# Kernel optimization log

Hardware: AMD Instinct MI355X
Metric: run time of the kernel (lower is better)

## Reference

```python
import jax, jax.numpy as jnp
import numpy as np

N = 100_000   # nodes
E = 1_600_000 # edges
F = 128       # node_feature_dim
H = 128       # hidden_dim
A = 32        # action_dim
G = 64        # graphs in batch


def setup_inputs() -> dict:
    key = jax.random.key(0)
    ks = jax.random.split(key, 12)
    s = 0.05
    return {
        "x": jax.random.normal(ks[0], (N, F), jnp.float32),
        "edge_index": jax.random.randint(ks[1], (2, E), 0, N, dtype=jnp.int32),
        "batch": jnp.sort(jax.random.randint(ks[2], (N,), 0, G, dtype=jnp.int32)),
        "W1": jax.random.normal(ks[3], (F, H), jnp.float32) * s,
        "b1": jnp.zeros((H,), jnp.float32),
        "W2": jax.random.normal(ks[4], (H, H), jnp.float32) * s,
        "b2": jnp.zeros((H,), jnp.float32),
        "Wa": jax.random.normal(ks[5], (H, A), jnp.float32) * s,
        "ba": jnp.zeros((A,), jnp.float32),
        "Wv": jax.random.normal(ks[6], (H, 1), jnp.float32) * s,
        "bv": jnp.zeros((1,), jnp.float32),
        "log_std": jnp.zeros((A,), jnp.float32),
    }


def reference(x, edge_index, batch, W1, b1, W2, b2, Wa, ba, Wv, bv, log_std):
    src, dst = edge_index[0], edge_index[1]
    # GCN symmetric norm with self-loops: deg_i = 1 + #incoming edges
    deg = jax.ops.segment_sum(jnp.ones((E,), x.dtype), dst, num_segments=N) + 1.0
    dinv = deg ** -0.5  # [N]

    def gcn(h, W, b):
        h = h @ W                                   # [N,H] dense transform first (as PyG GCNConv)
        msg = h[src] * dinv[src, None]              # gather + src norm
        agg = jax.ops.segment_sum(msg, dst, num_segments=N) * dinv[:, None]
        agg = agg + h * (dinv * dinv)[:, None]      # self-loop contribution
        return agg + b

    h = jax.nn.relu(gcn(x, W1, b1))
    h = jax.nn.relu(gcn(h, W2, b2))

    # global_mean_pool over graph segments
    counts = jax.ops.segment_sum(jnp.ones((N,), h.dtype), batch, num_segments=G)
    pooled = jax.ops.segment_sum(h, batch, num_segments=G) / jnp.maximum(counts, 1.0)[:, None]

    action_mean = pooled @ Wa + ba                  # [G,A]
    value = (pooled @ Wv + bv)[:, 0]                # [G]
    return action_mean, jnp.exp(log_std), value
```

## Files before the change

kernel.cpp:

```cpp
#include <hip/hip_runtime.h>
#include <hip/hip_bf16.h>

#define FDIM 128
#define HDIM 128
#define ADIM 32
#define BSH 6
#define BWD 64
#define CHUNK 8192
#define MAXNB 2048
#define CSRCAP 2048

#define CP(p) ((((p) & 7) << 4) | ((p) >> 3))

typedef short v8s __attribute__((ext_vector_type(8)));
typedef float v4f __attribute__((ext_vector_type(4)));
typedef float v2f __attribute__((ext_vector_type(2)));

static __device__ __forceinline__ float bflo(unsigned int u) {
    return __builtin_bit_cast(float, u << 16);
}
static __device__ __forceinline__ float bfhi(unsigned int u) {
    return __builtin_bit_cast(float, u & 0xffff0000u);
}
static __device__ __forceinline__ unsigned int bfpack(float a, float b) {
    unsigned int ua = __builtin_bit_cast(unsigned int, a);
    unsigned int ub = __builtin_bit_cast(unsigned int, b);
    ua += 0x7fffu + ((ua >> 16) & 1u);
    ub += 0x7fffu + ((ub >> 16) & 1u);
    return (ua >> 16) | (ub & 0xffff0000u);
}

#if defined(__has_builtin) && __has_builtin(__builtin_amdgcn_cvt_pk_f32_fp8) && \
    __has_builtin(__builtin_amdgcn_cvt_pk_fp8_f32)
#define FP8_HW 1
#endif

static __device__ __forceinline__ v2f fp8_dec_lo(unsigned int u) {
#ifdef FP8_HW
    return __builtin_amdgcn_cvt_pk_f32_fp8(u, false);
#else
    v2f r;
    #pragma unroll
    for (int i = 0; i < 2; ++i) {
        unsigned b = (u >> (8 * i)) & 0xffu;
        unsigned s = b >> 7, e = (b >> 3) & 0xfu, m = b & 7u;
        float v = (e == 0) ? (float)m * 0.001953125f
                           : __builtin_bit_cast(float, ((e + 120u) << 23) | (m << 20));
        r[i] = s ? -v : v;
    }
    return r;
#endif
}
static __device__ __forceinline__ v2f fp8_dec_hi(unsigned int u) {
#ifdef FP8_HW
    return __builtin_amdgcn_cvt_pk_f32_fp8(u, true);
#else
    return fp8_dec_lo(u >> 16);
#endif
}

#ifndef FP8_HW
static __device__ __forceinline__ unsigned int fp8_enc1(float x) {
    unsigned s = __builtin_bit_cast(unsigned, x) >> 31;
    float ax = fabsf(x);
    if (ax > 448.f) return (s << 7) | 0x7Eu;
    if (ax < 0.0009765625f) return s << 7;
    int e2 = (int)((__builtin_bit_cast(unsigned, ax) >> 23) & 0xff) - 127;
    int qe = (e2 < -6 ? -6 : e2) - 3;
    float q = __builtin_bit_cast(float, (unsigned)((qe + 127) << 23));
    float r = rintf(ax / q) * q;
    if (r > 448.f) return (s << 7) | 0x7Eu;
    if (r < 0.001953125f) return s << 7;
    unsigned ub = __builtin_bit_cast(unsigned, r);
    int re = (int)((ub >> 23) & 0xff) - 127;
    if (re < -6) {
        unsigned m = (unsigned)rintf(r * 512.f);
        return (s << 7) | m;
    }
    return (s << 7) | ((unsigned)(re + 7) << 3) | ((ub >> 20) & 7u);
}
#endif

static __device__ __forceinline__ unsigned int fp8x4_enc(float a, float b, float c, float d) {
#ifdef FP8_HW
    int p = __builtin_amdgcn_cvt_pk_fp8_f32(a, b, 0, false);
    p = __builtin_amdgcn_cvt_pk_fp8_f32(c, d, p, true);
    return (unsigned int)p;
#else
    return fp8_enc1(a) | (fp8_enc1(b) << 8) | (fp8_enc1(c) << 16) | (fp8_enc1(d) << 24);
#endif
}

__global__ __launch_bounds__(256) void block_hist_setup(const int* __restrict__ dst,
                                                        int* __restrict__ hist,
                                                        int E, int NB, int NBLK,
                                                        const float* __restrict__ W1,
                                                        const float* __restrict__ W2,
                                                        const float* __restrict__ b1,
                                                        const float* __restrict__ b2,
                                                        unsigned short* __restrict__ wsw1,
                                                        unsigned short* __restrict__ wsw2,
                                                        float* __restrict__ pb1,
                                                        float* __restrict__ pb2,
                                                        const int* __restrict__ batch,
                                                        int* __restrict__ gstart,
                                                        float* __restrict__ pooled,
                                                        unsigned int* __restrict__ zrow,
                                                        int n, int G) {
    __shared__ int h[MAXNB];
    const int tid = threadIdx.x;
    if (blockIdx.x >= (unsigned)NBLK) {
        const int role = blockIdx.x - NBLK;
        if (role == 0) {
            for (int idx = tid; idx < 16384; idx += 256) {
                int nn = idx >> 7, k = idx & 127;
                wsw1[idx] = (unsigned short)(bfpack(W1[k * 128 + nn], 0.f) & 0xffffu);
                wsw2[idx] = (unsigned short)(bfpack(W2[CP(k) * 128 + nn], 0.f) & 0xffffu);
            }
            if (tid < 128) {
                pb1[tid] = b1[CP(tid)];
                pb2[tid] = b2[CP(tid)];
            }
        } else if (role == 1) {
            if (tid <= G) {
                int lo = 0, hi = n;
                while (lo < hi) { int mid = (lo + hi) >> 1; if (batch[mid] < tid) lo = mid + 1; else hi = mid; }
                gstart[tid] = lo;
            }
        } else {
            for (int i = tid; i < G * 128; i += 256) pooled[i] = 0.f;
            if (tid < 32) zrow[tid] = 0u;
        }
        return;
    }
    for (int i = tid; i < NB; i += 256) h[i] = 0;
    __syncthreads();
    const int base = blockIdx.x * CHUNK;
    int lim = base + CHUNK; if (lim > E) lim = E;
    for (int i = base + tid; i < lim; i += 256) atomicAdd(&h[dst[i] >> BSH], 1);
    __syncthreads();
    int* hrow = hist + (size_t)blockIdx.x * NB;
    for (int b = tid; b < NB; b += 256) hrow[b] = h[b];
}

__global__ void scanA(const int* __restrict__ hist, int* __restrict__ excl,
                      int* __restrict__ bsum, int M, int NB, int NBLK) {
    __shared__ int tmp[256];
    const int t = threadIdx.x;
    const int idx = blockIdx.x * 2048 + t * 8;
    int v[8], s = 0;
    #pragma unroll
    for (int i = 0; i < 8; ++i) {
        int p = idx + i;
        v[i] = (p < M) ? hist[(size_t)(p % NBLK) * NB + (p / NBLK)] : 0;
        s += v[i];
    }
    tmp[t] = s;
    __syncthreads();
    for (int off = 1; off < 256; off <<= 1) {
        int x = (t >= off) ? tmp[t - off] : 0;
        __syncthreads();
        tmp[t] += x;
        __syncthreads();
    }
    int run = tmp[t] - s;
    #pragma unroll
    for (int i = 0; i < 8; ++i) {
        int p = idx + i;
        if (p < M) excl[p] = run;
        run += v[i];
    }
    if (t == 255) bsum[blockIdx.x] = tmp[255];
}

__global__ void scanB(int* __restrict__ bsum, int nb) {
    __shared__ int tmp[256];
    const int t = threadIdx.x;
    int s = (t < nb) ? bsum[t] : 0;
    tmp[t] = s;
    __syncthreads();
    for (int off = 1; off < 256; off <<= 1) {
        int x = (t >= off) ? tmp[t - off] : 0;
        __syncthreads();
        tmp[t] += x;
        __syncthreads();
    }
    if (t < nb) bsum[t] = tmp[t] - s;
}

__global__ __launch_bounds__(256) void bucket_scatter(const int* __restrict__ src,
                                                      const int* __restrict__ dst,
                                                      const int* __restrict__ excl,
                                                      const int* __restrict__ bsum,
                                                      unsigned int* __restrict__ packed,
                                                      int E, int NB, int NBLK) {
    __shared__ int cur[MAXNB];
    const int tid = threadIdx.x;
    const int blk = blockIdx.x;
    for (int b = tid; b < NB; b += 256) {
        size_t p = (size_t)b * NBLK + blk;
        cur[b] = excl[p] + bsum[p >> 11];
    }
    __syncthreads();
    const int base = blk * CHUNK;
    int lim = base + CHUNK; if (lim > E) lim = E;
    for (int i = base + tid; i < lim; i += 256) {
        int d = dst[i];
        int s = src[i];
        int pos = atomicAdd(&cur[d >> BSH], 1);
        packed[pos] = (unsigned)s | ((unsigned)(d & (BWD - 1)) << 26);
    }
}

__global__ __launch_bounds__(256) void bucket_to_csr(const unsigned int* __restrict__ packed,
                                                     const int* __restrict__ excl,
                                                     const int* __restrict__ bsum,
                                                     int* __restrict__ rowptr,
                                                     int* __restrict__ pdeg,
                                                     float* __restrict__ dinv,
                                                     int* __restrict__ col,
                                                     int E, int N, int NB, int NBLK) {
    __shared__ int cnt[BWD];
    __shared__ int offs[BWD];
    __shared__ int ovf;
    const int b = blockIdx.x;
    const int tid = threadIdx.x;
    size_t p0 = (size_t)b * NBLK;
    const int base = excl[p0] + bsum[p0 >> 11];
    int next;
    if (b + 1 < NB) {
        size_t p1 = (size_t)(b + 1) * NBLK;
        next = excl[p1] + bsum[p1 >> 11];
    } else {
        next = E;
    }
    if (tid < BWD) cnt[tid] = 0;
    if (tid == 0) ovf = 0;
    __syncthreads();
    for (int i = base + tid; i < next; i += 256) atomicAdd(&cnt[packed[i] >> 26], 1);
    __syncthreads();
    const int rc = (tid < BWD) ? cnt[tid] : 0;
    if (tid == 0) {
        int run = 0;
        for (int j = 0; j < BWD; ++j) { offs[j] = run; run += (cnt[j] + 7) & ~7; }
        if (run > CSRCAP) {
            ovf = 1;
            run = 0;
            for (int j = 0; j < BWD; ++j) { offs[j] = run; run += cnt[j]; }
        }
    }
    __syncthreads();
    const int cbase = b * CSRCAP;
    if (tid < BWD) {
        int node = (b << BSH) + tid;
        if (node < N) {
            int pd = ovf ? rc : ((rc + 7) & ~7);
            int st = cbase + offs[tid];
            rowptr[node] = st;
            pdeg[node] = pd;
            dinv[node] = rsqrtf((float)rc + 1.0f);
            for (int k = rc; k < pd; ++k) col[st + k] = N;
        }
        cnt[tid] = offs[tid];
    }
    __syncthreads();
    for (int i = base + tid; i < next; i += 256) {
        unsigned int u = packed[i];
        int j = u >> 26;
        int pos = cbase + atomicAdd(&cnt[j], 1);
        col[pos] = (int)(u & 0x03ffffffu);
    }
}

template <bool BF16IN>
__global__ __launch_bounds__(256, 4) void gemm_mfma(const void* __restrict__ Xv,
                                                    const unsigned short* __restrict__ wsw,
                                                    const float* __restrict__ rowscale,
                                                    uint2* __restrict__ Out, int n) {
    __shared__ char sW[32768];
    const int tid = threadIdx.x;
    const int w = tid >> 6;
    const int lane = tid & 63;
    const int q = lane >> 4;
    const int m15 = lane & 15;
    const int rbase = blockIdx.x * 64;

    const int arow = rbase + w * 16 + m15;
    const int srow = (arow < n) ? arow : (n - 1);

    uint4 ta[4];
    float4 tf[8];
    if (BF16IN) {
        const unsigned short* xr = (const unsigned short*)Xv + (size_t)srow * 128 + q * 8;
        #pragma unroll
        for (int kk = 0; kk < 4; ++kk) ta[kk] = *(const uint4*)(xr + kk * 32);
    } else {
        const float* xr = (const float*)Xv + (size_t)srow * 128 + q * 8;
        #pragma unroll
        for (int kk = 0; kk < 4; ++kk) {
            tf[2 * kk]     = *(const float4*)(xr + kk * 32);
            tf[2 * kk + 1] = *(const float4*)(xr + kk * 32 + 4);
        }
    }

    #pragma unroll
    for (int it = 0; it < 8; ++it) {
        int fi = it * 256 + tid;
        uint4 v = ((const uint4*)wsw)[fi];
        *(uint4*)(sW + ((fi * 16) ^ (((fi >> 4) & 7) << 4))) = v;
    }
    __syncthreads();

    v8s a[4];
    if (BF16IN) {
        #pragma unroll
        for (int kk = 0; kk < 4; ++kk) a[kk] = __builtin_bit_cast(v8s, ta[kk]);
    } else {
        #pragma unroll
        for (int kk = 0; kk < 4; ++kk) {
            uint4 p;
            p.x = bfpack(tf[2 * kk].x, tf[2 * kk].y);
            p.y = bfpack(tf[2 * kk].z, tf[2 * kk].w);
            p.z = bfpack(tf[2 * kk + 1].x, tf[2 * kk + 1].y);
            p.w = bfpack(tf[2 * kk + 1].z, tf[2 * kk + 1].w);
            a[kk] = __builtin_bit_cast(v8s, p);
        }
    }

    const int swz = (m15 & 7) << 4;
    v8s bcur[4], bnxt[4];
    #pragma unroll
    for (int kk = 0; kk < 4; ++kk)
        bcur[kk] = *(const v8s*)(sW + (((m15 * 16 + kk * 4 + q) * 16) ^ swz));

    v4f acc[8];
    #pragma unroll
    for (int nt = 0; nt < 8; ++nt) acc[nt] = (v4f){0.f, 0.f, 0.f, 0.f};

    #pragma unroll
    for (int nt = 0; nt < 8; ++nt) {
        if (nt < 7) {
            #pragma unroll
            for (int kk = 0; kk < 4; ++kk)
                bnxt[kk] = *(const v8s*)(sW +
                    (((((nt + 1) * 16 + m15) * 16 + kk * 4 + q) * 16) ^ swz));
        }
        #pragma unroll
        for (int kk = 0; kk < 4; ++kk)
            acc[nt] = __builtin_amdgcn_mfma_f32_16x16x32_bf16(a[kk], bcur[kk], acc[nt], 0, 0, 0);
        #pragma unroll
        for (int kk = 0; kk < 4; ++kk) bcur[kk] = bnxt[kk];
    }

    #pragma unroll
    for (int reg = 0; reg < 4; ++reg) {
        int row = rbase + w * 16 + q * 4 + reg;
        if (row < n) {
            float sc = rowscale[row];
            unsigned int d0 = fp8x4_enc(acc[0][reg] * sc, acc[1][reg] * sc,
                                        acc[2][reg] * sc, acc[3][reg] * sc);
            unsigned int d1 = fp8x4_enc(acc[4][reg] * sc, acc[5][reg] * sc,
                                        acc[6][reg] * sc, acc[7][reg] * sc);
            Out[(size_t)row * 16 + m15] = make_uint2(d0, d1);
        }
    }
}

__global__ __launch_bounds__(256) void gather_fused(const unsigned int* __restrict__ T32,
                                                    const int* __restrict__ rowptr,
                                                    const int* __restrict__ pdeg,
                                                    const int* __restrict__ col,
                                                    const float* __restrict__ dinv,
                                                    const float* __restrict__ pbias,
                                                    uint2* __restrict__ H, int n) {
    const int wave = (blockIdx.x * 256 + threadIdx.x) >> 6;
    const int d = wave * 2 + ((threadIdx.x >> 5) & 1);
    const int hl = threadIdx.x & 31;
    if (d >= n) return;
    int e = rowptr[d];
    const int end = e + pdeg[d];

    v2f sl0 = {0.f, 0.f}, sh0 = {0.f, 0.f}, sl1 = {0.f, 0.f}, sh1 = {0.f, 0.f};

    if ((e & 1) && e < end) {
        unsigned int u = T32[(size_t)col[e] * 32 + hl];
        sl0 += fp8_dec_lo(u); sh0 += fp8_dec_hi(u);
        ++e;
    }
    for (; e + 7 < end; e += 8) {
        int2 p01 = *(const int2*)(col + e);
        int2 p23 = *(const int2*)(col + e + 2);
        int2 p45 = *(const int2*)(col + e + 4);
        int2 p67 = *(const int2*)(col + e + 6);
        unsigned int u0 = T32[(size_t)p01.x * 32 + hl];
        unsigned int u1 = T32[(size_t)p01.y * 32 + hl];
        unsigned int u2 = T32[(size_t)p23.x * 32 + hl];
        unsigned int u3 = T32[(size_t)p23.y * 32 + hl];
        unsigned int u4 = T32[(size_t)p45.x * 32 + hl];
        unsigned int u5 = T32[(size_t)p45.y * 32 + hl];
        unsigned int u6 = T32[(size_t)p67.x * 32 + hl];
        unsigned int u7 = T32[(size_t)p67.y * 32 + hl];
        sl0 += fp8_dec_lo(u0); sh0 += fp8_dec_hi(u0);
        sl1 += fp8_dec_lo(u1); sh1 += fp8_dec_hi(u1);
        sl0 += fp8_dec_lo(u2); sh0 += fp8_dec_hi(u2);
        sl1 += fp8_dec_lo(u3); sh1 += fp8_dec_hi(u3);
        sl0 += fp8_dec_lo(u4); sh0 += fp8_dec_hi(u4);
        sl1 += fp8_dec_lo(u5); sh1 += fp8_dec_hi(u5);
        sl0 += fp8_dec_lo(u6); sh0 += fp8_dec_hi(u6);
        sl1 += fp8_dec_lo(u7); sh1 += fp8_dec_hi(u7);
    }
    for (; e + 1 < end; e += 2) {
        int2 p = *(const int2*)(col + e);
        unsigned int u0 = T32[(size_t)p.x * 32 + hl];
        unsigned int u1 = T32[(size_t)p.y * 32 + hl];
        sl0 += fp8_dec_lo(u0); sh0 += fp8_dec_hi(u0);
        sl1 += fp8_dec_lo(u1); sh1 += fp8_dec_hi(u1);
    }
    if (e < end) {
        unsigned int u = T32[(size_t)col[e] * 32 + hl];
        sl0 += fp8_dec_lo(u); sh0 += fp8_dec_hi(u);
    }

    unsigned int su = T32[(size_t)d * 32 + hl];
    sl0 += fp8_dec_lo(su); sh0 += fp8_dec_hi(su);
    v2f sl = sl0 + sl1, sh = sh0 + sh1;

    const float di = dinv[d];
    const float4 bv = ((const float4*)pbias)[hl];
    float o0 = fmaxf(fmaf(sl.x, di, bv.x), 0.f);
    float o1 = fmaxf(fmaf(sl.y, di, bv.y), 0.f);
    float o2 = fmaxf(fmaf(sh.x, di, bv.z), 0.f);
    float o3 = fmaxf(fmaf(sh.y, di, bv.w), 0.f);
    uint2 o;
    o.x = bfpack(o0, o1);
    o.y = bfpack(o2, o3);
    H[(size_t)d * 32 + hl] = o;
}

__global__ __launch_bounds__(256) void gather_pool(const unsigned int* __restrict__ T32,
                                                   const int* __restrict__ rowptr,
                                                   const int* __restrict__ pdeg,
                                                   const int* __restrict__ col,
                                                   const float* __restrict__ dinv,
                                                   const float* __restrict__ pbias,
                                                   float* __restrict__ pooled,
                                                   const int* __restrict__ batch,
                                                   int n) {
    __shared__ float pacc[256];
    const int tid = threadIdx.x;
    const int hw = tid >> 5;
    const int hl = tid & 31;
    const int base = blockIdx.x * 64;
    pacc[tid] = 0.f;
    const int g0 = batch[base < n ? base : (n - 1)];
    __syncthreads();

    const float4 bv = ((const float4*)pbias)[hl];
    float r0a = 0.f, r0b = 0.f, r0c = 0.f, r0d = 0.f;
    float r1a = 0.f, r1b = 0.f, r1c = 0.f, r1d = 0.f;

    for (int it = 0; it < 8; ++it) {
        const int d = base + hw * 8 + it;
        if (d < n) {
            int e = rowptr[d];
            const int end = e + pdeg[d];

            v2f sl0 = {0.f, 0.f}, sh0 = {0.f, 0.f}, sl1 = {0.f, 0.f}, sh1 = {0.f, 0.f};

            if ((e & 1) && e < end) {
                unsigned int u = T32[(size_t)col[e] * 32 + hl];
                sl0 += fp8_dec_lo(u); sh0 += fp8_dec_hi(u);
                ++e;
            }
            for (; e + 7 < end; e += 8) {
                int2 p01 = *(const int2*)(col + e);
                int2 p23 = *(const int2*)(col + e + 2);
                int2 p45 = *(const int2*)(col + e + 4);
                int2 p67 = *(const int2*)(col + e + 6);
                unsigned int u0 = T32[(size_t)p01.x * 32 + hl];
                unsigned int u1 = T32[(size_t)p01.y * 32 + hl];
                unsigned int u2 = T32[(size_t)p23.x * 32 + hl];
                unsigned int u3 = T32[(size_t)p23.y * 32 + hl];
                unsigned int u4 = T32[(size_t)p45.x * 32 + hl];
                unsigned int u5 = T32[(size_t)p45.y * 32 + hl];
                unsigned int u6 = T32[(size_t)p67.x * 32 + hl];
                unsigned int u7 = T32[(size_t)p67.y * 32 + hl];
                sl0 += fp8_dec_lo(u0); sh0 += fp8_dec_hi(u0);
                sl1 += fp8_dec_lo(u1); sh1 += fp8_dec_hi(u1);
                sl0 += fp8_dec_lo(u2); sh0 += fp8_dec_hi(u2);
                sl1 += fp8_dec_lo(u3); sh1 += fp8_dec_hi(u3);
                sl0 += fp8_dec_lo(u4); sh0 += fp8_dec_hi(u4);
                sl1 += fp8_dec_lo(u5); sh1 += fp8_dec_hi(u5);
                sl0 += fp8_dec_lo(u6); sh0 += fp8_dec_hi(u6);
                sl1 += fp8_dec_lo(u7); sh1 += fp8_dec_hi(u7);
            }
            for (; e + 1 < end; e += 2) {
                int2 p = *(const int2*)(col + e);
                unsigned int u0 = T32[(size_t)p.x * 32 + hl];
                unsigned int u1 = T32[(size_t)p.y * 32 + hl];
                sl0 += fp8_dec_lo(u0); sh0 += fp8_dec_hi(u0);
                sl1 += fp8_dec_lo(u1); sh1 += fp8_dec_hi(u1);
            }
            if (e < end) {
                unsigned int u = T32[(size_t)col[e] * 32 + hl];
                sl0 += fp8_dec_lo(u); sh0 += fp8_dec_hi(u);
            }

            unsigned int su = T32[(size_t)d * 32 + hl];
            sl0 += fp8_dec_lo(su); sh0 += fp8_dec_hi(su);
            v2f sl = sl0 + sl1, sh = sh0 + sh1;

            const float di = dinv[d];
            float o0 = fmaxf(fmaf(sl.x, di, bv.x), 0.f);
            float o1 = fmaxf(fmaf(sl.y, di, bv.y), 0.f);
            float o2 = fmaxf(fmaf(sh.x, di, bv.z), 0.f);
            float o3 = fmaxf(fmaf(sh.y, di, bv.w), 0.f);

            const int gi = batch[d] - g0;
            if (gi == 0) {
                r0a += o0; r0b += o1; r0c += o2; r0d += o3;
            } else if (gi == 1) {
                r1a += o0; r1b += o1; r1c += o2; r1d += o3;
            } else {
                atomicAdd(&pooled[(size_t)(g0 + gi) * 128 + 4 * hl + 0], o0);
                atomicAdd(&pooled[(size_t)(g0 + gi) * 128 + 4 * hl + 1], o1);
                atomicAdd(&pooled[(size_t)(g0 + gi) * 128 + 4 * hl + 2], o2);
                atomicAdd(&pooled[(size_t)(g0 + gi) * 128 + 4 * hl + 3], o3);
            }
        }
    }

    atomicAdd(&pacc[4 * hl + 0], r0a);
    atomicAdd(&pacc[4 * hl + 1], r0b);
    atomicAdd(&pacc[4 * hl + 2], r0c);
    atomicAdd(&pacc[4 * hl + 3], r0d);
    if (r1a != 0.f || r1b != 0.f || r1c != 0.f || r1d != 0.f) {
        atomicAdd(&pacc[128 + 4 * hl + 0], r1a);
        atomicAdd(&pacc[128 + 4 * hl + 1], r1b);
        atomicAdd(&pacc[128 + 4 * hl + 2], r1c);
        atomicAdd(&pacc[128 + 4 * hl + 3], r1d);
    }
    __syncthreads();
    float v = pacc[tid];
    if (v != 0.f) {
        int gg = g0 + (tid >> 7);
        atomicAdd(&pooled[(size_t)gg * 128 + (tid & 127)], v);
    }
}

__global__ void head_kernel(const float* __restrict__ pooled, const int* __restrict__ gstart,
                            const float* __restrict__ Wa, const float* __restrict__ ba,
                            const float* __restrict__ Wv, const float* __restrict__ bv,
                            const float* __restrict__ log_std, float* __restrict__ out, int G) {
    int g = blockIdx.x;
    int t = threadIdx.x;
    __shared__ float sp[128];
    float inv = 1.0f / fmaxf((float)(gstart[g + 1] - gstart[g]), 1.0f);
    sp[t] = pooled[(size_t)g * 128 + t] * inv;
    sp[t + 64] = pooled[(size_t)g * 128 + 64 + t] * inv;
    __syncthreads();
    if (t < 32) {
        float s = 0.f;
        #pragma unroll 8
        for (int k = 0; k < 128; ++k) s = fmaf(sp[k], Wa[CP(k) * ADIM + t], s);
        out[g * ADIM + t] = s + ba[t];
        if (g == 0) out[G * ADIM + t] = expf(log_std[t]);
    } else if (t == 32) {
        float s = 0.f;
        #pragma unroll 8
        for (int k = 0; k < 128; ++k) s = fmaf(sp[k], Wv[CP(k)], s);
        out[G * ADIM + ADIM + g] = s + bv[0];
    }
}

extern "C" void kernel_launch(void* const* d_in, const int* in_sizes, int n_in,
                              void* d_out, int out_size, void* d_ws, size_t ws_size,
                              hipStream_t stream) {
    const float* x       = (const float*)d_in[0];
    const int*   ei      = (const int*)d_in[1];
    const int*   batch   = (const int*)d_in[2];
    const float* W1      = (const float*)d_in[3];
    const float* b1      = (const float*)d_in[4];
    const float* W2      = (const float*)d_in[5];
    const float* b2      = (const float*)d_in[6];
    const float* Wa      = (const float*)d_in[7];
    const float* ba      = (const float*)d_in[8];
    const float* Wv      = (const float*)d_in[9];
    const float* bv      = (const float*)d_in[10];
    const float* log_std = (const float*)d_in[11];
    float* out = (float*)d_out;

    const int N = in_sizes[0] / FDIM;
    const int E = in_sizes[1] / 2;
    const int G = (out_size - ADIM) / (ADIM + 1);
    const int NB = (N + BWD - 1) >> BSH;
    const int NBLK = (E + CHUNK - 1) / CHUNK;
    const int M = NB * NBLK;
    const int nscanA = (M + 2047) / 2048;

    const int* src = ei;
    const int* dst = ei + E;

    auto align = [](size_t v) { return (v + 255) & ~(size_t)255; };
    char* ws = (char*)d_ws;
    size_t off = 0;
    int*   hist   = (int*)(ws + off);   off = align(off + (size_t)M * 4);
    int*   excl   = (int*)(ws + off);   off = align(off + (size_t)M * 4);
    int*   bsum   = (int*)(ws + off);   off = align(off + (size_t)256 * 4);
    int*   rowptr = (int*)(ws + off);   off = align(off + (size_t)(N + 1) * 4);
    int*   pdeg   = (int*)(ws + off);   off = align(off + (size_t)N * 4);
    int*   gstart = (int*)(ws + off);   off = align(off + (size_t)(G + 1) * 4);
    float* dinv   = (float*)(ws + off); off = align(off + (size_t)N * 4);
    float* pooled = (float*)(ws + off); off = align(off + (size_t)G * HDIM * 4);
    unsigned short* wsw1 = (unsigned short*)(ws + off); off = align(off + (size_t)16384 * 2);
    unsigned short* wsw2 = (unsigned short*)(ws + off); off = align(off + (size_t)16384 * 2);
    float* pb1    = (float*)(ws + off); off = align(off + (size_t)128 * 4);
    float* pb2    = (float*)(ws + off); off = align(off + (size_t)128 * 4);
    unsigned int* packed = (unsigned int*)(ws + off); off = align(off + (size_t)E * 4);
    int*   col    = (int*)(ws + off);   off = align(off + (size_t)NB * CSRCAP * 4);
    unsigned int* bufA = (unsigned int*)(ws + off); off = align(off + (size_t)(N + 1) * 32 * 4);
    unsigned int* bufB = (unsigned int*)(ws + off); off = align(off + (size_t)N * 64 * 4);
    (void)ws_size;

    unsigned int* zrow = bufA + (size_t)N * 32;

    const int blkGemm = (N + 63) / 64;
    const int blkGather = (N + 7) / 8;
    const int blkGP = (N + 63) / 64;

    block_hist_setup<<<NBLK + 3, 256, 0, stream>>>(dst, hist, E, NB, NBLK,
                                                   W1, W2, b1, b2, wsw1, wsw2, pb1, pb2,
                                                   batch, gstart, pooled, zrow, N, G);
    scanA<<<nscanA, 256, 0, stream>>>(hist, excl, bsum, M, NB, NBLK);
    scanB<<<1, 256, 0, stream>>>(bsum, nscanA);
    bucket_scatter<<<NBLK, 256, 0, stream>>>(src, dst, excl, bsum, packed, E, NB, NBLK);
    bucket_to_csr<<<NB, 256, 0, stream>>>(packed, excl, bsum, rowptr, pdeg, dinv, col, E, N, NB, NBLK);

    gemm_mfma<false><<<blkGemm, 256, 0, stream>>>(x, wsw1, dinv, (uint2*)bufA, N);
    gather_fused<<<blkGather, 256, 0, stream>>>(bufA, rowptr, pdeg, col, dinv, pb1,
                                                (uint2*)bufB, N);

    gemm_mfma<true><<<blkGemm, 256, 0, stream>>>(bufB, wsw2, dinv, (uint2*)bufA, N);
    gather_pool<<<blkGP, 256, 0, stream>>>(bufA, rowptr, pdeg, col, dinv, pb2,
                                           pooled, batch, N);

    head_kernel<<<G, 64, 0, stream>>>(pooled, gstart, Wa, ba, Wv, bv, log_std, out, G);
}
```

Measured before the change: 263.3 us.

## Fold block-sum scan into consumers and fuse head into pooling via last-block

Removes the single-block scanB launch by having each bucket_scatter and bucket_to_csr block redundantly scan the small bsum array in shared memory. Removes the separate head_kernel launch by having the last block to finish gather_pool, detected with an atomic done counter, compute the action-mean and value heads. The goal is to save two kernel launches and their inter-kernel gaps. In exchange every block repeats a 256-element scan, and the head work runs serially in a single block at the tail of gather_pool.

```diff
diff --git a/kernel.cpp b/kernel.cpp
--- a/kernel.cpp
+++ b/kernel.cpp
@@ -106,6 +106,7 @@
                                                         int* __restrict__ gstart,
                                                         float* __restrict__ pooled,
                                                         unsigned int* __restrict__ zrow,
+                                                        int* __restrict__ donecnt,
                                                         int n, int G) {
     __shared__ int h[MAXNB];
     const int tid = threadIdx.x;
@@ -130,6 +131,7 @@
         } else {
             for (int i = tid; i < G * 128; i += 256) pooled[i] = 0.f;
             if (tid < 32) zrow[tid] = 0u;
+            if (tid == 0) donecnt[0] = 0;
         }
         return;
     }
@@ -173,19 +175,22 @@
     if (t == 255) bsum[blockIdx.x] = tmp[255];
 }
 
-__global__ void scanB(int* __restrict__ bsum, int nb) {
-    __shared__ int tmp[256];
+static __device__ __forceinline__ void local_bscan(const int* __restrict__ bsum,
+                                                   int nscan, int* bscan) {
     const int t = threadIdx.x;
-    int s = (t < nb) ? bsum[t] : 0;
-    tmp[t] = s;
+    int s0 = (t < nscan) ? bsum[t] : 0;
+    bscan[t] = s0;
     __syncthreads();
     for (int off = 1; off < 256; off <<= 1) {
-        int x = (t >= off) ? tmp[t - off] : 0;
+        int x = (t >= off) ? bscan[t - off] : 0;
         __syncthreads();
-        tmp[t] += x;
+        bscan[t] += x;
         __syncthreads();
     }
-    if (t < nb) bsum[t] = tmp[t] - s;
+    int ex = bscan[t] - s0;
+    __syncthreads();
+    bscan[t] = ex;
+    __syncthreads();
 }
 
 __global__ __launch_bounds__(256) void bucket_scatter(const int* __restrict__ src,
@@ -193,13 +198,15 @@
                                                       const int* __restrict__ excl,
                                                       const int* __restrict__ bsum,
                                                       unsigned int* __restrict__ packed,
-                                                      int E, int NB, int NBLK) {
+                                                      int E, int NB, int NBLK, int nscan) {
     __shared__ int cur[MAXNB];
+    __shared__ int bscan[256];
     const int tid = threadIdx.x;
     const int blk = blockIdx.x;
+    local_bscan(bsum, nscan, bscan);
     for (int b = tid; b < NB; b += 256) {
         size_t p = (size_t)b * NBLK + blk;
-        cur[b] = excl[p] + bsum[p >> 11];
+        cur[b] = excl[p] + bscan[p >> 11];
     }
     __syncthreads();
     const int base = blk * CHUNK;
@@ -219,18 +226,20 @@
                                                      int* __restrict__ pdeg,
                                                      float* __restrict__ dinv,
                                                      int* __restrict__ col,
-                                                     int E, int N, int NB, int NBLK) {
+                                                     int E, int N, int NB, int NBLK, int nscan) {
     __shared__ int cnt[BWD];
     __shared__ int offs[BWD];
     __shared__ int ovf;
+    __shared__ int bscan[256];
     const int b = blockIdx.x;
     const int tid = threadIdx.x;
+    local_bscan(bsum, nscan, bscan);
     size_t p0 = (size_t)b * NBLK;
-    const int base = excl[p0] + bsum[p0 >> 11];
+    const int base = excl[p0] + bscan[p0 >> 11];
     int next;
     if (b + 1 < NB) {
         size_t p1 = (size_t)(b + 1) * NBLK;
-        next = excl[p1] + bsum[p1 >> 11];
+        next = excl[p1] + bscan[p1 >> 11];
     } else {
         next = E;
     }
@@ -445,7 +454,15 @@
                                                    const float* __restrict__ pbias,
                                                    float* __restrict__ pooled,
                                                    const int* __restrict__ batch,
-                                                   int n) {
+                                                   int* __restrict__ donecnt,
+                                                   const int* __restrict__ gstart,
+                                                   const float* __restrict__ Wa,
+                                                   const float* __restrict__ ba,
+                                                   const float* __restrict__ Wv,
+                                                   const float* __restrict__ bv2,
+                                                   const float* __restrict__ log_std,
+                                                   float* __restrict__ out,
+                                                   int n, int G) {
     __shared__ float pacc[256];
     const int tid = threadIdx.x;
     const int hw = tid >> 5;
@@ -546,31 +563,34 @@
         int gg = g0 + (tid >> 7);
         atomicAdd(&pooled[(size_t)gg * 128 + (tid & 127)], v);
     }
-}
-
-__global__ void head_kernel(const float* __restrict__ pooled, const int* __restrict__ gstart,
-                            const float* __restrict__ Wa, const float* __restrict__ ba,
-                            const float* __restrict__ Wv, const float* __restrict__ bv,
-                            const float* __restrict__ log_std, float* __restrict__ out, int G) {
-    int g = blockIdx.x;
-    int t = threadIdx.x;
-    __shared__ float sp[128];
-    float inv = 1.0f / fmaxf((float)(gstart[g + 1] - gstart[g]), 1.0f);
-    sp[t] = pooled[(size_t)g * 128 + t] * inv;
-    sp[t + 64] = pooled[(size_t)g * 128 + 64 + t] * inv;
-    __syncthreads();
-    if (t < 32) {
-        float s = 0.f;
+
+    __threadfence();
+    __syncthreads();
+    __shared__ int lastv;
+    if (tid == 0) lastv = (atomicAdd(donecnt, 1) == (int)gridDim.x - 1);
+    __syncthreads();
+    if (!lastv) return;
+    __threadfence();
+
+    __shared__ float sp8[8][128];
+    const int grp = tid >> 5;
+    const int l32 = tid & 31;
+    for (int g = grp; g < G; g += 8) {
+        float inv = 1.0f / fmaxf((float)(gstart[g + 1] - gstart[g]), 1.0f);
+        for (int k = l32; k < 128; k += 32)
+            sp8[grp][k] = __hip_atomic_load(&pooled[(size_t)g * 128 + k],
+                                            __ATOMIC_RELAXED, __HIP_MEMORY_SCOPE_AGENT) * inv;
+        float sa = 0.f;
         #pragma unroll 8
-        for (int k = 0; k < 128; ++k) s = fmaf(sp[k], Wa[CP(k) * ADIM + t], s);
-        out[g * ADIM + t] = s + ba[t];
-        if (g == 0) out[G * ADIM + t] = expf(log_std[t]);
-    } else if (t == 32) {
-        float s = 0.f;
-        #pragma unroll 8
-        for (int k = 0; k < 128; ++k) s = fmaf(sp[k], Wv[CP(k)], s);
-        out[G * ADIM + ADIM + g] = s + bv[0];
-    }
+        for (int k = 0; k < 128; ++k) sa = fmaf(sp8[grp][k], Wa[CP(k) * ADIM + l32], sa);
+        out[g * ADIM + l32] = sa + ba[l32];
+        float pv = 0.f;
+        for (int k = l32; k < 128; k += 32) pv = fmaf(sp8[grp][k], Wv[CP(k)], pv);
+        #pragma unroll
+        for (int o = 16; o; o >>= 1) pv += __shfl_down(pv, o, 32);
+        if (l32 == 0) out[G * ADIM + ADIM + g] = pv + bv2[0];
+    }
+    if (tid < ADIM) out[G * ADIM + tid] = expf(log_std[tid]);
 }
 
 extern "C" void kernel_launch(void* const* d_in, const int* in_sizes, int n_in,
@@ -612,6 +632,7 @@
     int*   gstart = (int*)(ws + off);   off = align(off + (size_t)(G + 1) * 4);
     float* dinv   = (float*)(ws + off); off = align(off + (size_t)N * 4);
     float* pooled = (float*)(ws + off); off = align(off + (size_t)G * HDIM * 4);
+    int*   donecnt = (int*)(ws + off);  off = align(off + (size_t)16 * 4);
     unsigned short* wsw1 = (unsigned short*)(ws + off); off = align(off + (size_t)16384 * 2);
     unsigned short* wsw2 = (unsigned short*)(ws + off); off = align(off + (size_t)16384 * 2);
     float* pb1    = (float*)(ws + off); off = align(off + (size_t)128 * 4);
@@ -630,11 +651,11 @@
 
     block_hist_setup<<<NBLK + 3, 256, 0, stream>>>(dst, hist, E, NB, NBLK,
                                                    W1, W2, b1, b2, wsw1, wsw2, pb1, pb2,
-                                                   batch, gstart, pooled, zrow, N, G);
+                                                   batch, gstart, pooled, zrow, donecnt, N, G);
     scanA<<<nscanA, 256, 0, stream>>>(hist, excl, bsum, M, NB, NBLK);
-    scanB<<<1, 256, 0, stream>>>(bsum, nscanA);
-    bucket_scatter<<<NBLK, 256, 0, stream>>>(src, dst, excl, bsum, packed, E, NB, NBLK);
-    bucket_to_csr<<<NB, 256, 0, stream>>>(packed, excl, bsum, rowptr, pdeg, dinv, col, E, N, NB, NBLK);
+    bucket_scatter<<<NBLK, 256, 0, stream>>>(src, dst, excl, bsum, packed, E, NB, NBLK, nscanA);
+    bucket_to_csr<<<NB, 256, 0, stream>>>(packed, excl, bsum, rowptr, pdeg, dinv, col,
+                                          E, N, NB, NBLK, nscanA);
 
     gemm_mfma<false><<<blkGemm, 256, 0, stream>>>(x, wsw1, dinv, (uint2*)bufA, N);
     gather_fused<<<blkGather, 256, 0, stream>>>(bufA, rowptr, pdeg, col, dinv, pb1,
@@ -642,7 +663,6 @@
 
     gemm_mfma<true><<<blkGemm, 256, 0, stream>>>(bufB, wsw2, dinv, (uint2*)bufA, N);
     gather_pool<<<blkGP, 256, 0, stream>>>(bufA, rowptr, pdeg, col, dinv, pb2,
-                                           pooled, batch, N);
-
-    head_kernel<<<G, 64, 0, stream>>>(pooled, gstart, Wa, ba, Wv, bv, log_std, out, G);
-}
+                                           pooled, batch, donecnt,
+                                           gstart, Wa, ba, Wv, bv, log_std, out, N, G);
+}
```

After: 419.7 us. 1.59x slower.
